# Performance work log

Hardware: AMD Instinct MI355X
Metric: run time of the kernel (lower is better)

## Reference

```python
import jax, jax.numpy as jnp
import numpy as np

B, H, S, D = 4, 16, 2048, 64

def setup_inputs() -> dict:
    key = jax.random.key(0)
    kq, kk, kv = jax.random.split(key, 3)
    q = jax.random.normal(kq, (B, H, S, D), dtype=jnp.float32)
    k = jax.random.normal(kk, (B, H, S, D), dtype=jnp.float32)
    v = jax.random.normal(kv, (B, H, S, D), dtype=jnp.float32)
    return {"q": q, "k": k, "v": v}

def reference(q, k, v):
    # Based linear attention: Taylor-expanded exp kernel, causal, row-sum normalized.
    d = q.shape[-1]
    scale = 1.0 / jnp.sqrt(jnp.asarray(d, dtype=q.dtype))
    s = jnp.einsum('bhqd,bhkd->bhqk', q, k) * scale          # [B,H,S,S]
    p = 1.0 + s + 0.5 * (s * s)                               # Taylor exp approx
    seq = s.shape[-1]
    causal = jnp.tril(jnp.ones((seq, seq), dtype=bool))       # [S,S]
    p = jnp.where(causal, p, 0.0)
    denom = jnp.sum(p, axis=-1, keepdims=True) + 1e-6         # [B,H,S,1]
    out = jnp.einsum('bhqk,bhkd->bhqd', p, v) / denom
    return out
```

## Files before the change

kernel.cpp:

```cpp
#include <hip/hip_runtime.h>
#include <hip/hip_bf16.h>

#define S_LEN 2048
#define DH    64
#define QB    128
#define KB    64
#define BHN   64
#define NQT   16
#define LDS_STRIDE 72

typedef __attribute__((ext_vector_type(8))) short short8;
typedef __attribute__((ext_vector_type(4))) float f32x4;

union Frag {
  short8   s;
  unsigned u[4];
};

__device__ __forceinline__ unsigned pack2(float a, float b) {
  __hip_bfloat162 h2 = __float22bfloat162_rn(make_float2(a, b));
  unsigned u; __builtin_memcpy(&u, &h2, 4);
  return u;
}

__global__ __launch_bounds__(256, 2)
void repack(const float* __restrict__ Kg, const float* __restrict__ Vg,
            short* __restrict__ ws) {
  const int bt = blockIdx.x;
  const int tid = threadIdx.x;
  const size_t tilebase = (size_t)bt * (64 * 64);
  short* kout = ws + (size_t)bt * 4096;
  short* vout = ws + 8388608 + (size_t)bt * 4096;

#pragma unroll
  for (int it = 0; it < 2; ++it) {
    const int c2 = tid + it * 256;
    const int f = c2 >> 6, l = c2 & 63;
    const int kkh = f >> 2, hi = (f >> 1) & 1, cc = f & 1;
    const int row = kkh * 32 + hi * 16 + (l & 15);
    const int col = cc * 32 + (l >> 4) * 8;
    const float* src = Kg + tilebase + row * 64 + col;
    float4 a = *(const float4*)src, b = *(const float4*)(src + 4);
    Frag w;
    w.u[0] = pack2(a.x, a.y); w.u[1] = pack2(a.z, a.w);
    w.u[2] = pack2(b.x, b.y); w.u[3] = pack2(b.z, b.w);
    *(short8*)(kout + f * 512 + l * 8) = w.s;
  }

  __shared__ float vt[64 * 65];
#pragma unroll
  for (int it = 0; it < 4; ++it) {
    const int i = tid + it * 256;
    const int r = i >> 4, c4 = i & 15;
    float4 x = *(const float4*)(Vg + tilebase + r * 64 + c4 * 4);
    vt[r * 65 + c4 * 4 + 0] = x.x; vt[r * 65 + c4 * 4 + 1] = x.y;
    vt[r * 65 + c4 * 4 + 2] = x.z; vt[r * 65 + c4 * 4 + 3] = x.w;
  }
  __syncthreads();
#pragma unroll
  for (int it = 0; it < 2; ++it) {
    const int v2 = tid + it * 256;
    const int v = v2 >> 6, l = v2 & 63;
    const int kkh = v >> 2, n = v & 3;
    const int d = n * 16 + (l & 15);
    const int k0c = kkh * 32 + (l >> 4) * 8;
    Frag w;
#pragma unroll
    for (int jj = 0; jj < 4; ++jj)
      w.u[jj] = pack2(vt[(k0c + 2 * jj) * 65 + d], vt[(k0c + 2 * jj + 1) * 65 + d]);
    *(short8*)(vout + v * 512 + l * 8) = w.s;
  }
}

#define GLOAD(t_, T0, T1, T2, T3)                                              \
  do {                                                                         \
    const short* gsrc_ = ((wv < 2) ? Kf : Vf)                                  \
                         + ((size_t)((bh << 5) + (t_)) << 12)                  \
                         + (size_t)((wv & 1) * 4) * 512 + lane * 8;            \
    T0 = *(const short8*)(gsrc_ + 0 * 512);                                    \
    T1 = *(const short8*)(gsrc_ + 1 * 512);                                    \
    T2 = *(const short8*)(gsrc_ + 2 * 512);                                    \
    T3 = *(const short8*)(gsrc_ + 3 * 512);                                    \
  } while (0)

#define DSWRITE(t_, T0, T1, T2, T3)                                            \
  do {                                                                         \
    short* ld_ = &ring[((t_) & 3) * 8192 + ((wv >= 2) ? 4096 : 0)              \
                       + ((wv & 1) * 4) * 512 + lane * 8];                     \
    *(short8*)(ld_ + 0 * 512) = T0;                                            \
    *(short8*)(ld_ + 1 * 512) = T1;                                            \
    *(short8*)(ld_ + 2 * 512) = T2;                                            \
    *(short8*)(ld_ + 3 * 512) = T3;                                            \
  } while (0)

#define COMPUTE_LDS(t_, MASKED_)                                               \
  do {                                                                         \
    const short* tb_ = &ring[((t_) & 3) * 8192];                               \
    short8 kfr[8], vfr[8];                                                     \
    _Pragma("unroll")                                                          \
    for (int f = 0; f < 8; ++f) kfr[f] = *(const short8*)(tb_ + f * 512 + lane * 8); \
    _Pragma("unroll")                                                          \
    for (int f = 0; f < 8; ++f) vfr[f] = *(const short8*)(tb_ + 4096 + f * 512 + lane * 8); \
    const int k0_ = (t_) * KB;                                                 \
    _Pragma("unroll")                                                          \
    for (int kkh = 0; kkh < 2; ++kkh) {                                        \
      const int kk = kkh * 32;                                                 \
      if (!(MASKED_) || (q0 + wv * 32 + 31 >= k0_ + kk)) {                     \
        f32x4 stL[2], stH[2];                                                  \
        _Pragma("unroll")                                                      \
        for (int hq = 0; hq < 2; ++hq) {                                       \
          stL[hq] = (f32x4){0.f, 0.f, 0.f, 0.f};                               \
          stH[hq] = (f32x4){0.f, 0.f, 0.f, 0.f};                               \
          _Pragma("unroll")                                                    \
          for (int c = 0; c < 2; ++c) {                                        \
            stL[hq] = __builtin_amdgcn_mfma_f32_16x16x32_bf16(kfr[kkh * 4 + c],     qf[hq][c].s, stL[hq], 0, 0, 0); \
            stH[hq] = __builtin_amdgcn_mfma_f32_16x16x32_bf16(kfr[kkh * 4 + 2 + c], qf[hq][c].s, stH[hq], 0, 0, 0); \
          }                                                                    \
        }                                                                      \
        unsigned wrd[2][4];                                                    \
        _Pragma("unroll")                                                      \
        for (int hq = 0; hq < 2; ++hq) {                                       \
          const int qrow = q0 + wv * 32 + hq * 16 + qid;                       \
          float pl[4], ph[4];                                                  \
          _Pragma("unroll")                                                    \
          for (int r = 0; r < 4; ++r) {                                        \
            float sl = stL[hq][r], sh = stH[hq][r];                            \
            pl[r] = fmaf(sl, fmaf(sl, 0.5f, 1.0f), 1.0f);                      \
            ph[r] = fmaf(sh, fmaf(sh, 0.5f, 1.0f), 1.0f);                      \
            if (MASKED_) {                                                     \
              if (k0_ + kk + 4 * g + r > qrow)      pl[r] = 0.f;               \
              if (k0_ + kk + 16 + 4 * g + r > qrow) ph[r] = 0.f;               \
            }                                                                  \
          }                                                                    \
          wrd[hq][0] = pack2(pl[0], pl[1]);                                    \
          wrd[hq][1] = pack2(pl[2], pl[3]);                                    \
          wrd[hq][2] = pack2(ph[0], ph[1]);                                    \
          wrd[hq][3] = pack2(ph[2], ph[3]);                                    \
        }                                                                      \
        Frag pa[2];                                                            \
        _Pragma("unroll")                                                      \
        for (int hq = 0; hq < 2; ++hq) {                                       \
          auto sA32 = __builtin_amdgcn_permlane32_swap(wrd[hq][0], wrd[hq][2], false, false); \
          auto sA16 = __builtin_amdgcn_permlane16_swap(sA32[0], sA32[1], false, false);       \
          auto sB32 = __builtin_amdgcn_permlane32_swap(wrd[hq][1], wrd[hq][3], false, false); \
          auto sB16 = __builtin_amdgcn_permlane16_swap(sB32[0], sB32[1], false, false);       \
          pa[hq].u[0] = (unsigned)sA16[0];                                     \
          pa[hq].u[2] = (unsigned)sA16[1];                                     \
          pa[hq].u[1] = (unsigned)sB16[0];                                     \
          pa[hq].u[3] = (unsigned)sB16[1];                                     \
        }                                                                      \
        _Pragma("unroll")                                                      \
        for (int n = 0; n < 4; ++n) {                                          \
          acc[0][n] = __builtin_amdgcn_mfma_f32_16x16x32_bf16(pa[0].s, vfr[kkh * 4 + n], acc[0][n], 0, 0, 0); \
          acc[1][n] = __builtin_amdgcn_mfma_f32_16x16x32_bf16(pa[1].s, vfr[kkh * 4 + n], acc[1][n], 0, 0, 0); \
        }                                                                      \
        dacc[0] = __builtin_amdgcn_mfma_f32_16x16x32_bf16(pa[0].s, ones.s, dacc[0], 0, 0, 0); \
        dacc[1] = __builtin_amdgcn_mfma_f32_16x16x32_bf16(pa[1].s, ones.s, dacc[1], 0, 0, 0); \
      }                                                                        \
    }                                                                          \
  } while (0)

__global__ __launch_bounds__(256, 2)
void based_lds(const float* __restrict__ Qg, const short* __restrict__ Fr,
               float* __restrict__ Og) {
  const int tid  = threadIdx.x;
  const int lane = tid & 63;
  const int wv   = tid >> 6;
  const int qid  = lane & 15;
  const int g    = lane >> 4;

  const int bh = blockIdx.x;
  const int qy = blockIdx.y;

  __shared__ __align__(16) short ring[4 * 8192];

  const short* Kf = Fr;
  const short* Vf = Fr + 8388608;
  const size_t base = (size_t)bh * S_LEN;

  Frag ones;
  {
    const unsigned ov = (qid == 0) ? 0x3F803F80u : 0u;
    ones.u[0] = ov; ones.u[1] = ov; ones.u[2] = ov; ones.u[3] = ov;
  }

  short8 a0, a1, a2, a3;
  short8 b0, b1, b2, b3;
  short8 c0, c1, c2, c3;

#pragma unroll 1
  for (int half = 0; half < 2; ++half) {
    const int qt = half ? (NQT - 1 - qy) : qy;
    const int q0 = qt * QB;

    Frag qf[2][2];
    {
      const float SC = 0.125f;
#pragma unroll
      for (int hq = 0; hq < 2; ++hq) {
        const int qrow = q0 + wv * 32 + hq * 16 + qid;
        const float* qp = Qg + (base + qrow) * DH + g * 8;
#pragma unroll
        for (int c = 0; c < 2; ++c) {
          float4 f0 = *(const float4*)(qp + c * 32);
          float4 f1 = *(const float4*)(qp + c * 32 + 4);
          qf[hq][c].u[0] = pack2(f0.x * SC, f0.y * SC);
          qf[hq][c].u[1] = pack2(f0.z * SC, f0.w * SC);
          qf[hq][c].u[2] = pack2(f1.x * SC, f1.y * SC);
          qf[hq][c].u[3] = pack2(f1.z * SC, f1.w * SC);
        }
      }
    }

    f32x4 acc[2][4];
    f32x4 dacc[2];
#pragma unroll
    for (int hq = 0; hq < 2; ++hq) {
      dacc[hq] = (f32x4){0.f, 0.f, 0.f, 0.f};
#pragma unroll
      for (int n = 0; n < 4; ++n) acc[hq][n] = (f32x4){0.f, 0.f, 0.f, 0.f};
    }

    const int nfull = 2 * qt;
    const int nt    = nfull + 2;

    __syncthreads();
    GLOAD(0, a0, a1, a2, a3);
    GLOAD(1, b0, b1, b2, b3);
    if (nt > 2) GLOAD(2, c0, c1, c2, c3);
    DSWRITE(0, a0, a1, a2, a3);
    DSWRITE(1, b0, b1, b2, b3);
    if (nt > 2) DSWRITE(2, c0, c1, c2, c3);
    __syncthreads();

    for (int t = 0; t < nfull; ++t) {
      const bool st = (t + 3 < nt);
      if (st) GLOAD(t + 3, a0, a1, a2, a3);
      COMPUTE_LDS(t, 0);
      if (st) DSWRITE(t + 3, a0, a1, a2, a3);
      __syncthreads();
    }

    COMPUTE_LDS(nfull, 1);
    COMPUTE_LDS(nfull + 1, 1);

#pragma unroll
    for (int hq = 0; hq < 2; ++hq) {
#pragma unroll
      for (int r = 0; r < 4; ++r) {
        float dn  = __shfl(dacc[hq][r], 16 * g);
        float inv = 1.0f / (dn + 1e-6f);
        const int row = q0 + wv * 32 + hq * 16 + 4 * g + r;
        float* op = Og + (base + row) * DH + qid;
#pragma unroll
        for (int n = 0; n < 4; ++n) op[n * 16] = acc[hq][n][r] * inv;
      }
    }
  }
}

#define STAGE_LOAD(k0_)                                                        \
  do {                                                                         \
    if (tid < 128) {                                                           \
      const float4* ksrc = (const float4*)(Kg + (base + (size_t)(k0_)) * DH); \
      r0 = ksrc[tid];       r1 = ksrc[tid + 128];                              \
      r2 = ksrc[tid + 256]; r3 = ksrc[tid + 384];                              \
      r4 = ksrc[tid + 512]; r5 = ksrc[tid + 640];                              \
      r6 = ksrc[tid + 768]; r7 = ksrc[tid + 896];                              \
    } else {                                                                   \
      const float4* vsrc = (const float4*)(Vg + (base + (size_t)(k0_)) * DH)  \
                           + ((tid - 128) >> 4) * 128 + ((tid - 128) & 15);    \
      r0 = vsrc[0];  r1 = vsrc[16]; r2 = vsrc[32]; r3 = vsrc[48];              \
      r4 = vsrc[64]; r5 = vsrc[80]; r6 = vsrc[96]; r7 = vsrc[112];             \
    }                                                                          \
  } while (0)

#define STAGE_WRITE(b_)                                                        \
  do {                                                                         \
    if (tid < 128) {                                                           \
      short* Kd = Klds[b_];                                                    \
      const int rb = tid >> 4, c4 = tid & 15;                                  \
      *(uint2*)&Kd[(rb + 0)  * LDS_STRIDE + c4 * 4] = make_uint2(pack2(r0.x, r0.y), pack2(r0.z, r0.w)); \
      *(uint2*)&Kd[(rb + 8)  * LDS_STRIDE + c4 * 4] = make_uint2(pack2(r1.x, r1.y), pack2(r1.z, r1.w)); \
      *(uint2*)&Kd[(rb + 16) * LDS_STRIDE + c4 * 4] = make_uint2(pack2(r2.x, r2.y), pack2(r2.z, r2.w)); \
      *(uint2*)&Kd[(rb + 24) * LDS_STRIDE + c4 * 4] = make_uint2(pack2(r3.x, r3.y), pack2(r3.z, r3.w)); \
      *(uint2*)&Kd[(rb + 32) * LDS_STRIDE + c4 * 4] = make_uint2(pack2(r4.x, r4.y), pack2(r4.z, r4.w)); \
      *(uint2*)&Kd[(rb + 40) * LDS_STRIDE + c4 * 4] = make_uint2(pack2(r5.x, r5.y), pack2(r5.z, r5.w)); \
      *(uint2*)&Kd[(rb + 48) * LDS_STRIDE + c4 * 4] = make_uint2(pack2(r6.x, r6.y), pack2(r6.z, r6.w)); \
      *(uint2*)&Kd[(rb + 56) * LDS_STRIDE + c4 * 4] = make_uint2(pack2(r7.x, r7.y), pack2(r7.z, r7.w)); \
    } else {                                                                   \
      short* Vd = Vlds[b_];                                                    \
      const int l = tid - 128, c4 = l & 15, rp = l >> 4;                       \
      const int slot = (rp + (c4 & 7)) & 7;                                    \
      short* vp = &Vd[(c4 * 4) * LDS_STRIDE + slot * 8];                       \
      Frag w;                                                                  \
      w.u[0] = pack2(r0.x, r1.x); w.u[1] = pack2(r2.x, r3.x);                  \
      w.u[2] = pack2(r4.x, r5.x); w.u[3] = pack2(r6.x, r7.x);                  \
      *(short8*)&vp[0 * LDS_STRIDE] = w.s;                                     \
      w.u[0] = pack2(r0.y, r1.y); w.u[1] = pack2(r2.y, r3.y);                  \
      w.u[2] = pack2(r4.y, r5.y); w.u[3] = pack2(r6.y, r7.y);                  \
      *(short8*)&vp[1 * LDS_STRIDE] = w.s;                                     \
      w.u[0] = pack2(r0.z, r1.z); w.u[1] = pack2(r2.z, r3.z);                  \
      w.u[2] = pack2(r4.z, r5.z); w.u[3] = pack2(r6.z, r7.z);                  \
      *(short8*)&vp[2 * LDS_STRIDE] = w.s;                                     \
      w.u[0] = pack2(r0.w, r1.w); w.u[1] = pack2(r2.w, r3.w);                  \
      w.u[2] = pack2(r4.w, r5.w); w.u[3] = pack2(r6.w, r7.w);                  \
      *(short8*)&vp[3 * LDS_STRIDE] = w.s;                                     \
    }                                                                          \
  } while (0)

#define COMPUTE_TILE(KbP_, VbP_, k0_, MASKED_)                                 \
  do {                                                                         \
    const short* Kb = (KbP_);                                                  \
    const short* Vb = (VbP_);                                                  \
    _Pragma("unroll")                                                          \
    for (int kk = 0; kk < KB; kk += 32) {                                      \
      if (!(MASKED_) || (q0 + wv * 32 + 31 >= (k0_) + kk)) {                   \
        short8 aLo[2], aHi[2];                                                 \
        _Pragma("unroll")                                                      \
        for (int c = 0; c < 2; ++c) {                                          \
          aLo[c] = *(const short8*)&Kb[(kk + qid) * LDS_STRIDE + c * 32 + g * 8];        \
          aHi[c] = *(const short8*)&Kb[(kk + 16 + qid) * LDS_STRIDE + c * 32 + g * 8];   \
        }                                                                      \
        f32x4 stL[2], stH[2];                                                  \
        _Pragma("unroll")                                                      \
        for (int hq = 0; hq < 2; ++hq) {                                       \
          stL[hq] = (f32x4){0.f, 0.f, 0.f, 0.f};                               \
          stH[hq] = (f32x4){0.f, 0.f, 0.f, 0.f};                               \
          _Pragma("unroll")                                                    \
          for (int c = 0; c < 2; ++c) {                                        \
            stL[hq] = __builtin_amdgcn_mfma_f32_16x16x32_bf16(aLo[c], qf[hq][c].s, stL[hq], 0, 0, 0); \
            stH[hq] = __builtin_amdgcn_mfma_f32_16x16x32_bf16(aHi[c], qf[hq][c].s, stH[hq], 0, 0, 0); \
          }                                                                    \
        }                                                                      \
        unsigned wrd[2][4];                                                    \
        _Pragma("unroll")                                                      \
        for (int hq = 0; hq < 2; ++hq) {                                       \
          const int qrow = q0 + wv * 32 + hq * 16 + qid;                       \
          float pl[4], ph[4];                                                  \
          _Pragma("unroll")                                                    \
          for (int r = 0; r < 4; ++r) {                                        \
            float sl = stL[hq][r], sh = stH[hq][r];                            \
            pl[r] = fmaf(sl, fmaf(sl, 0.5f, 1.0f), 1.0f);                      \
            ph[r] = fmaf(sh, fmaf(sh, 0.5f, 1.0f), 1.0f);                      \
            if (MASKED_) {                                                     \
              if ((k0_) + kk + 4 * g + r > qrow)      pl[r] = 0.f;             \
              if ((k0_) + kk + 16 + 4 * g + r > qrow) ph[r] = 0.f;             \
            }                                                                  \
          }                                                                    \
          wrd[hq][0] = pack2(pl[0], pl[1]);                                    \
          wrd[hq][1] = pack2(pl[2], pl[3]);                                    \
          wrd[hq][2] = pack2(ph[0], ph[1]);                                    \
          wrd[hq][3] = pack2(ph[2], ph[3]);                                    \
        }                                                                      \
        Frag pa[2];                                                            \
        _Pragma("unroll")                                                      \
        for (int hq = 0; hq < 2; ++hq) {                                       \
          auto sA32 = __builtin_amdgcn_permlane32_swap(wrd[hq][0], wrd[hq][2], false, false); \
          auto sA16 = __builtin_amdgcn_permlane16_swap(sA32[0], sA32[1], false, false);       \
          auto sB32 = __builtin_amdgcn_permlane32_swap(wrd[hq][1], wrd[hq][3], false, false); \
          auto sB16 = __builtin_amdgcn_permlane16_swap(sB32[0], sB32[1], false, false);       \
          pa[hq].u[0] = (unsigned)sA16[0];                                     \
          pa[hq].u[2] = (unsigned)sA16[1];                                     \
          pa[hq].u[1] = (unsigned)sB16[0];                                     \
          pa[hq].u[3] = (unsigned)sB16[1];                                     \
        }                                                                      \
        _Pragma("unroll")                                                      \
        for (int n = 0; n < 4; ++n) {                                          \
          const int row = n * 16 + qid;                                        \
          const int un  = ((kk >> 3) + g + ((row >> 2) & 7)) & 7;              \
          short8 vb = *(const short8*)&Vb[row * LDS_STRIDE + un * 8];          \
          acc[0][n] = __builtin_amdgcn_mfma_f32_16x16x32_bf16(pa[0].s, vb, acc[0][n], 0, 0, 0); \
          acc[1][n] = __builtin_amdgcn_mfma_f32_16x16x32_bf16(pa[1].s, vb, acc[1][n], 0, 0, 0); \
        }                                                                      \
        dacc[0] = __builtin_amdgcn_mfma_f32_16x16x32_bf16(pa[0].s, ones.s, dacc[0], 0, 0, 0);   \
        dacc[1] = __builtin_amdgcn_mfma_f32_16x16x32_bf16(pa[1].s, ones.s, dacc[1], 0, 0, 0);   \
      }                                                                        \
    }                                                                          \
  } while (0)

__global__ __launch_bounds__(256, 2)
void based_attn(const float* __restrict__ Qg,
                const float* __restrict__ Kg,
                const float* __restrict__ Vg,
                float* __restrict__ Og) {
  const int tid  = threadIdx.x;
  const int lane = tid & 63;
  const int wv   = tid >> 6;
  const int qid  = lane & 15;
  const int g    = lane >> 4;

  const int bh = blockIdx.x;
  const int qy = blockIdx.y;

  __shared__ short Klds[2][KB * LDS_STRIDE];
  __shared__ short Vlds[2][DH * LDS_STRIDE];

  const size_t base = (size_t)bh * S_LEN;

  Frag ones;
  {
    const unsigned ov = (qid == 0) ? 0x3F803F80u : 0u;
    ones.u[0] = ov; ones.u[1] = ov; ones.u[2] = ov; ones.u[3] = ov;
  }

  float4 r0, r1, r2, r3, r4, r5, r6, r7;

#pragma unroll 1
  for (int half = 0; half < 2; ++half) {
    const int qt = half ? (NQT - 1 - qy) : qy;
    const int q0 = qt * QB;

    Frag qf[2][2];
    {
      const float SC = 0.125f;
#pragma unroll
      for (int hq = 0; hq < 2; ++hq) {
        const int qrow = q0 + wv * 32 + hq * 16 + qid;
        const float* qp = Qg + (base + qrow) * DH + g * 8;
#pragma unroll
        for (int c = 0; c < 2; ++c) {
          float4 f0 = *(const float4*)(qp + c * 32);
          float4 f1 = *(const float4*)(qp + c * 32 + 4);
          qf[hq][c].u[0] = pack2(f0.x * SC, f0.y * SC);
          qf[hq][c].u[1] = pack2(f0.z * SC, f0.w * SC);
          qf[hq][c].u[2] = pack2(f1.x * SC, f1.y * SC);
          qf[hq][c].u[3] = pack2(f1.z * SC, f1.w * SC);
        }
      }
    }

    f32x4 acc[2][4];
    f32x4 dacc[2];
#pragma unroll
    for (int hq = 0; hq < 2; ++hq) {
      dacc[hq] = (f32x4){0.f, 0.f, 0.f, 0.f};
#pragma unroll
      for (int n = 0; n < 4; ++n) acc[hq][n] = (f32x4){0.f, 0.f, 0.f, 0.f};
    }

    STAGE_LOAD(0);
    STAGE_WRITE(0);
    __syncthreads();

    const int nfull = 2 * qt;
    for (int t = 0; t < nfull; ++t) {
      STAGE_LOAD((t + 1) * KB);
      COMPUTE_TILE(Klds[t & 1], Vlds[t & 1], t * KB, 0);
      STAGE_WRITE((t + 1) & 1);
      __syncthreads();
    }
    {
      int t = nfull;
      STAGE_LOAD((t + 1) * KB);
      COMPUTE_TILE(Klds[t & 1], Vlds[t & 1], t * KB, 1);
      STAGE_WRITE((t + 1) & 1);
      __syncthreads();
      t = nfull + 1;
      COMPUTE_TILE(Klds[t & 1], Vlds[t & 1], t * KB, 1);
    }

#pragma unroll
    for (int hq = 0; hq < 2; ++hq) {
#pragma unroll
      for (int r = 0; r < 4; ++r) {
        float dn  = __shfl(dacc[hq][r], 16 * g);
        float inv = 1.0f / (dn + 1e-6f);
        const int row = q0 + wv * 32 + hq * 16 + 4 * g + r;
        float* op = Og + (base + row) * DH + qid;
#pragma unroll
        for (int n = 0; n < 4; ++n) op[n * 16] = acc[hq][n][r] * inv;
      }
    }
  }
}

extern "C" void kernel_launch(void* const* d_in, const int* in_sizes, int n_in,
                              void* d_out, int out_size, void* d_ws, size_t ws_size,
                              hipStream_t stream) {
  (void)in_sizes; (void)n_in; (void)out_size;
  const float* Q = (const float*)d_in[0];
  const float* K = (const float*)d_in[1];
  const float* V = (const float*)d_in[2];
  float* O = (float*)d_out;

  if (ws_size >= (size_t)33554432) {
    short* ws = (short*)d_ws;
    repack<<<dim3(2048), 256, 0, stream>>>(K, V, ws);
    based_lds<<<dim3(64, 8), 256, 0, stream>>>(Q, ws, O);
  } else {
    dim3 grid(BHN, NQT / 2);
    based_attn<<<grid, 256, 0, stream>>>(Q, K, V, O);
  }
}
```

Measured before the change: 69.53 us.

## Process paired low and high query tiles in one shared K/V sweep

Each block used to handle its two query tiles (qy and NQT-1-qy) one after the other, streaming the K/V prefix twice. Now both tiles' Q fragments and accumulators stay live together, so the K/V tiles for the low tile's range are loaded once and used by both tiles. This cuts repeated global and LDS traffic and pipeline refills. In exchange it roughly doubles accumulator and Q-fragment registers per wave, which may cause spills or lower occupancy under launch_bounds(256,2).

```diff
diff --git a/kernel.cpp b/kernel.cpp
--- a/kernel.cpp
+++ b/kernel.cpp
@@ -93,76 +93,97 @@
     *(short8*)(ld_ + 3 * 512) = T3;                                            \
   } while (0)
 
-#define COMPUTE_LDS(t_, MASKED_)                                               \
+#define QBODY(QF, ACC, DACC, Q0_, MASKED_)                                     \
+  if (!(MASKED_) || (Q0_ + wv * 32 + 31 >= k0_ + kk)) {                        \
+    f32x4 stL[2], stH[2];                                                      \
+    _Pragma("unroll")                                                          \
+    for (int hq = 0; hq < 2; ++hq) {                                           \
+      stL[hq] = (f32x4){0.f, 0.f, 0.f, 0.f};                                   \
+      stH[hq] = (f32x4){0.f, 0.f, 0.f, 0.f};                                   \
+      _Pragma("unroll")                                                        \
+      for (int c = 0; c < 2; ++c) {                                            \
+        stL[hq] = __builtin_amdgcn_mfma_f32_16x16x32_bf16(kf[c],     QF[hq][c].s, stL[hq], 0, 0, 0); \
+        stH[hq] = __builtin_amdgcn_mfma_f32_16x16x32_bf16(kf[2 + c], QF[hq][c].s, stH[hq], 0, 0, 0); \
+      }                                                                        \
+    }                                                                          \
+    unsigned wrd[2][4];                                                        \
+    _Pragma("unroll")                                                          \
+    for (int hq = 0; hq < 2; ++hq) {                                           \
+      const int qrow = Q0_ + wv * 32 + hq * 16 + qid;                          \
+      float pl[4], ph[4];                                                      \
+      _Pragma("unroll")                                                        \
+      for (int r = 0; r < 4; ++r) {                                            \
+        float sl = stL[hq][r], sh = stH[hq][r];                                \
+        pl[r] = fmaf(sl, fmaf(sl, 0.5f, 1.0f), 1.0f);                          \
+        ph[r] = fmaf(sh, fmaf(sh, 0.5f, 1.0f), 1.0f);                          \
+        if (MASKED_) {                                                         \
+          if (k0_ + kk + 4 * g + r > qrow)      pl[r] = 0.f;                   \
+          if (k0_ + kk + 16 + 4 * g + r > qrow) ph[r] = 0.f;                   \
+        }                                                                      \
+      }                                                                        \
+      wrd[hq][0] = pack2(pl[0], pl[1]);                                        \
+      wrd[hq][1] = pack2(pl[2], pl[3]);                                        \
+      wrd[hq][2] = pack2(ph[0], ph[1]);                                        \
+      wrd[hq][3] = pack2(ph[2], ph[3]);                                        \
+    }                                                                          \
+    Frag pa[2];                                                                \
+    _Pragma("unroll")                                                          \
+    for (int hq = 0; hq < 2; ++hq) {                                           \
+      auto sA32 = __builtin_amdgcn_permlane32_swap(wrd[hq][0], wrd[hq][2], false, false); \
+      auto sA16 = __builtin_amdgcn_permlane16_swap(sA32[0], sA32[1], false, false);       \
+      auto sB32 = __builtin_amdgcn_permlane32_swap(wrd[hq][1], wrd[hq][3], false, false); \
+      auto sB16 = __builtin_amdgcn_permlane16_swap(sB32[0], sB32[1], false, false);       \
+      pa[hq].u[0] = (unsigned)sA16[0];                                         \
+      pa[hq].u[2] = (unsigned)sA16[1];                                         \
+      pa[hq].u[1] = (unsigned)sB16[0];                                         \
+      pa[hq].u[3] = (unsigned)sB16[1];                                         \
+    }                                                                          \
+    _Pragma("unroll")                                                          \
+    for (int n = 0; n < 4; ++n) {                                              \
+      ACC[0][n] = __builtin_amdgcn_mfma_f32_16x16x32_bf16(pa[0].s, vf[n], ACC[0][n], 0, 0, 0); \
+      ACC[1][n] = __builtin_amdgcn_mfma_f32_16x16x32_bf16(pa[1].s, vf[n], ACC[1][n], 0, 0, 0); \
+    }                                                                          \
+    DACC[0] = __builtin_amdgcn_mfma_f32_16x16x32_bf16(pa[0].s, ones.s, DACC[0], 0, 0, 0); \
+    DACC[1] = __builtin_amdgcn_mfma_f32_16x16x32_bf16(pa[1].s, ones.s, DACC[1], 0, 0, 0); \
+  }
+
+#define PHASE(t_, DOLO, MLO, MHI)                                              \
   do {                                                                         \
     const short* tb_ = &ring[((t_) & 3) * 8192];                               \
-    short8 kfr[8], vfr[8];                                                     \
-    _Pragma("unroll")                                                          \
-    for (int f = 0; f < 8; ++f) kfr[f] = *(const short8*)(tb_ + f * 512 + lane * 8); \
-    _Pragma("unroll")                                                          \
-    for (int f = 0; f < 8; ++f) vfr[f] = *(const short8*)(tb_ + 4096 + f * 512 + lane * 8); \
     const int k0_ = (t_) * KB;                                                 \
     _Pragma("unroll")                                                          \
     for (int kkh = 0; kkh < 2; ++kkh) {                                        \
       const int kk = kkh * 32;                                                 \
-      if (!(MASKED_) || (q0 + wv * 32 + 31 >= k0_ + kk)) {                     \
-        f32x4 stL[2], stH[2];                                                  \
+      short8 kf[4], vf[4];                                                     \
+      _Pragma("unroll")                                                        \
+      for (int j = 0; j < 4; ++j) {                                            \
+        kf[j] = *(const short8*)(tb_ + (kkh * 4 + j) * 512 + lane * 8);        \
+        vf[j] = *(const short8*)(tb_ + 4096 + (kkh * 4 + j) * 512 + lane * 8); \
+      }                                                                        \
+      if (DOLO) { QBODY(qfL, accL, daccL, q0L, MLO) }                          \
+      QBODY(qfR, accR, daccR, q0R, MHI)                                        \
+    }                                                                          \
+  } while (0)
+
+#define EPI(ACC, DACC, Q0_)                                                    \
+  do {                                                                         \
+    _Pragma("unroll")                                                          \
+    for (int hq = 0; hq < 2; ++hq) {                                           \
+      _Pragma("unroll")                                                        \
+      for (int r = 0; r < 4; ++r) {                                            \
+        float dn  = __shfl(DACC[hq][r], 16 * g);                               \
+        float inv = 1.0f / (dn + 1e-6f);                                       \
+        const int row = Q0_ + wv * 32 + hq * 16 + 4 * g + r;                   \
+        float* op = Og + (base + row) * DH + qid;                              \
         _Pragma("unroll")                                                      \
-        for (int hq = 0; hq < 2; ++hq) {                                       \
-          stL[hq] = (f32x4){0.f, 0.f, 0.f, 0.f};                               \
-          stH[hq] = (f32x4){0.f, 0.f, 0.f, 0.f};                               \
-          _Pragma("unroll")                                                    \
-          for (int c = 0; c < 2; ++c) {                                        \
-            stL[hq] = __builtin_amdgcn_mfma_f32_16x16x32_bf16(kfr[kkh * 4 + c],     qf[hq][c].s, stL[hq], 0, 0, 0); \
-            stH[hq] = __builtin_amdgcn_mfma_f32_16x16x32_bf16(kfr[kkh * 4 + 2 + c], qf[hq][c].s, stH[hq], 0, 0, 0); \
-          }                                                                    \
-        }                                                                      \
-        unsigned wrd[2][4];                                                    \
-        _Pragma("unroll")                                                      \
-        for (int hq = 0; hq < 2; ++hq) {                                       \
-          const int qrow = q0 + wv * 32 + hq * 16 + qid;                       \
-          float pl[4], ph[4];                                                  \
-          _Pragma("unroll")                                                    \
-          for (int r = 0; r < 4; ++r) {                                        \
-            float sl = stL[hq][r], sh = stH[hq][r];                            \
-            pl[r] = fmaf(sl, fmaf(sl, 0.5f, 1.0f), 1.0f);                      \
-            ph[r] = fmaf(sh, fmaf(sh, 0.5f, 1.0f), 1.0f);                      \
-            if (MASKED_) {                                                     \
-              if (k0_ + kk + 4 * g + r > qrow)      pl[r] = 0.f;               \
-              if (k0_ + kk + 16 + 4 * g + r > qrow) ph[r] = 0.f;               \
-            }                                                                  \
-          }                                                                    \
-          wrd[hq][0] = pack2(pl[0], pl[1]);                                    \
-          wrd[hq][1] = pack2(pl[2], pl[3]);                                    \
-          wrd[hq][2] = pack2(ph[0], ph[1]);                                    \
-          wrd[hq][3] = pack2(ph[2], ph[3]);                                    \
-        }                                                                      \
-        Frag pa[2];                                                            \
-        _Pragma("unroll")                                                      \
-        for (int hq = 0; hq < 2; ++hq) {                                       \
-          auto sA32 = __builtin_amdgcn_permlane32_swap(wrd[hq][0], wrd[hq][2], false, false); \
-          auto sA16 = __builtin_amdgcn_permlane16_swap(sA32[0], sA32[1], false, false);       \
-          auto sB32 = __builtin_amdgcn_permlane32_swap(wrd[hq][1], wrd[hq][3], false, false); \
-          auto sB16 = __builtin_amdgcn_permlane16_swap(sB32[0], sB32[1], false, false);       \
-          pa[hq].u[0] = (unsigned)sA16[0];                                     \
-          pa[hq].u[2] = (unsigned)sA16[1];                                     \
-          pa[hq].u[1] = (unsigned)sB16[0];                                     \
-          pa[hq].u[3] = (unsigned)sB16[1];                                     \
-        }                                                                      \
-        _Pragma("unroll")                                                      \
-        for (int n = 0; n < 4; ++n) {                                          \
-          acc[0][n] = __builtin_amdgcn_mfma_f32_16x16x32_bf16(pa[0].s, vfr[kkh * 4 + n], acc[0][n], 0, 0, 0); \
-          acc[1][n] = __builtin_amdgcn_mfma_f32_16x16x32_bf16(pa[1].s, vfr[kkh * 4 + n], acc[1][n], 0, 0, 0); \
-        }                                                                      \
-        dacc[0] = __builtin_amdgcn_mfma_f32_16x16x32_bf16(pa[0].s, ones.s, dacc[0], 0, 0, 0); \
-        dacc[1] = __builtin_amdgcn_mfma_f32_16x16x32_bf16(pa[1].s, ones.s, dacc[1], 0, 0, 0); \
+        for (int n = 0; n < 4; ++n) op[n * 16] = ACC[hq][n][r] * inv;          \
       }                                                                        \
     }                                                                          \
   } while (0)
 
 __global__ __launch_bounds__(256, 2)
-void based_lds(const float* __restrict__ Qg, const short* __restrict__ Fr,
-               float* __restrict__ Og) {
+void based_dual(const float* __restrict__ Qg, const short* __restrict__ Fr,
+                float* __restrict__ Og) {
   const int tid  = threadIdx.x;
   const int lane = tid & 63;
   const int wv   = tid >> 6;
@@ -171,6 +192,8 @@
 
   const int bh = blockIdx.x;
   const int qy = blockIdx.y;
+  const int qlo = qy, qhi = NQT - 1 - qy;
+  const int q0L = qlo * QB, q0R = qhi * QB;
 
   __shared__ __align__(16) short ring[4 * 8192];
 
@@ -184,79 +207,83 @@
     ones.u[0] = ov; ones.u[1] = ov; ones.u[2] = ov; ones.u[3] = ov;
   }
 
-  short8 a0, a1, a2, a3;
-  short8 b0, b1, b2, b3;
-  short8 c0, c1, c2, c3;
-
-#pragma unroll 1
-  for (int half = 0; half < 2; ++half) {
-    const int qt = half ? (NQT - 1 - qy) : qy;
-    const int q0 = qt * QB;
-
-    Frag qf[2][2];
-    {
-      const float SC = 0.125f;
-#pragma unroll
-      for (int hq = 0; hq < 2; ++hq) {
-        const int qrow = q0 + wv * 32 + hq * 16 + qid;
+  Frag qfL[2][2], qfR[2][2];
+  {
+    const float SC = 0.125f;
+#pragma unroll
+    for (int hq = 0; hq < 2; ++hq) {
+#pragma unroll
+      for (int side = 0; side < 2; ++side) {
+        const int qrow = (side ? q0R : q0L) + wv * 32 + hq * 16 + qid;
         const float* qp = Qg + (base + qrow) * DH + g * 8;
 #pragma unroll
         for (int c = 0; c < 2; ++c) {
           float4 f0 = *(const float4*)(qp + c * 32);
           float4 f1 = *(const float4*)(qp + c * 32 + 4);
-          qf[hq][c].u[0] = pack2(f0.x * SC, f0.y * SC);
-          qf[hq][c].u[1] = pack2(f0.z * SC, f0.w * SC);
-          qf[hq][c].u[2] = pack2(f1.x * SC, f1.y * SC);
-          qf[hq][c].u[3] = pack2(f1.z * SC, f1.w * SC);
+          Frag w;
+          w.u[0] = pack2(f0.x * SC, f0.y * SC);
+          w.u[1] = pack2(f0.z * SC, f0.w * SC);
+          w.u[2] = pack2(f1.x * SC, f1.y * SC);
+          w.u[3] = pack2(f1.z * SC, f1.w * SC);
+          if (side) qfR[hq][c] = w; else qfL[hq][c] = w;
         }
       }
     }
-
-    f32x4 acc[2][4];
-    f32x4 dacc[2];
-#pragma unroll
-    for (int hq = 0; hq < 2; ++hq) {
-      dacc[hq] = (f32x4){0.f, 0.f, 0.f, 0.f};
-#pragma unroll
-      for (int n = 0; n < 4; ++n) acc[hq][n] = (f32x4){0.f, 0.f, 0.f, 0.f};
-    }
-
-    const int nfull = 2 * qt;
-    const int nt    = nfull + 2;
-
+  }
+
+  f32x4 accL[2][4], accR[2][4];
+  f32x4 daccL[2], daccR[2];
+#pragma unroll
+  for (int hq = 0; hq < 2; ++hq) {
+    daccL[hq] = (f32x4){0.f, 0.f, 0.f, 0.f};
+    daccR[hq] = (f32x4){0.f, 0.f, 0.f, 0.f};
+#pragma unroll
+    for (int n = 0; n < 4; ++n) {
+      accL[hq][n] = (f32x4){0.f, 0.f, 0.f, 0.f};
+      accR[hq][n] = (f32x4){0.f, 0.f, 0.f, 0.f};
+    }
+  }
+
+  const int nt = 2 * qhi + 2;
+  const int e1 = 2 * qlo, e2 = 2 * qlo + 2, e3 = 2 * qhi;
+
+  short8 a0, a1, a2, a3, b0, b1, b2, b3, c0, c1, c2, c3;
+
+  GLOAD(0, a0, a1, a2, a3);
+  GLOAD(1, b0, b1, b2, b3);
+  GLOAD(2, c0, c1, c2, c3);
+  DSWRITE(0, a0, a1, a2, a3);
+  DSWRITE(1, b0, b1, b2, b3);
+  DSWRITE(2, c0, c1, c2, c3);
+  __syncthreads();
+
+  int t = 0;
+  for (; t < e1; ++t) {
+    const bool st = (t + 3 < nt);
+    if (st) GLOAD(t + 3, a0, a1, a2, a3);
+    PHASE(t, 1, 0, 0);
+    if (st) DSWRITE(t + 3, a0, a1, a2, a3);
     __syncthreads();
-    GLOAD(0, a0, a1, a2, a3);
-    GLOAD(1, b0, b1, b2, b3);
-    if (nt > 2) GLOAD(2, c0, c1, c2, c3);
-    DSWRITE(0, a0, a1, a2, a3);
-    DSWRITE(1, b0, b1, b2, b3);
-    if (nt > 2) DSWRITE(2, c0, c1, c2, c3);
+  }
+  for (; t < e2; ++t) {
+    const bool st = (t + 3 < nt);
+    if (st) GLOAD(t + 3, a0, a1, a2, a3);
+    PHASE(t, 1, 1, 0);
+    if (st) DSWRITE(t + 3, a0, a1, a2, a3);
     __syncthreads();
-
-    for (int t = 0; t < nfull; ++t) {
-      const bool st = (t + 3 < nt);
-      if (st) GLOAD(t + 3, a0, a1, a2, a3);
-      COMPUTE_LDS(t, 0);
-      if (st) DSWRITE(t + 3, a0, a1, a2, a3);
-      __syncthreads();
-    }
-
-    COMPUTE_LDS(nfull, 1);
-    COMPUTE_LDS(nfull + 1, 1);
-
-#pragma unroll
-    for (int hq = 0; hq < 2; ++hq) {
-#pragma unroll
-      for (int r = 0; r < 4; ++r) {
-        float dn  = __shfl(dacc[hq][r], 16 * g);
-        float inv = 1.0f / (dn + 1e-6f);
-        const int row = q0 + wv * 32 + hq * 16 + 4 * g + r;
-        float* op = Og + (base + row) * DH + qid;
-#pragma unroll
-        for (int n = 0; n < 4; ++n) op[n * 16] = acc[hq][n][r] * inv;
-      }
-    }
-  }
+  }
+  EPI(accL, daccL, q0L);
+  for (; t < e3; ++t) {
+    const bool st = (t + 3 < nt);
+    if (st) GLOAD(t + 3, a0, a1, a2, a3);
+    PHASE(t, 0, 0, 0);
+    if (st) DSWRITE(t + 3, a0, a1, a2, a3);
+    __syncthreads();
+  }
+  for (; t < nt; ++t) {
+    PHASE(t, 0, 0, 1);
+  }
+  EPI(accR, daccR, q0R);
 }
 
 #define STAGE_LOAD(k0_)                                                        \
@@ -487,7 +514,7 @@
   if (ws_size >= (size_t)33554432) {
     short* ws = (short*)d_ws;
     repack<<<dim3(2048), 256, 0, stream>>>(K, V, ws);
-    based_lds<<<dim3(64, 8), 256, 0, stream>>>(Q, ws, O);
+    based_dual<<<dim3(64, 8), 256, 0, stream>>>(Q, ws, O);
   } else {
     dim3 grid(BHN, NQT / 2);
     based_attn<<<grid, 256, 0, stream>>>(Q, K, V, O);
```

After: 68.77 us. No clear change (-1.1%).

## Split attention into one query tile per block with double-buffered LDS ring

Applied to the files above, without the earlier changes.

Each block now handles a single causal query tile instead of a paired light and heavy tile. The grid doubles to 64x16, heaviest tiles are scheduled first, and launch bounds rise to 4 blocks per CU. The LDS ring shrinks from four tile slots to two, prefetch depth drops to one tile, and K/V fragments are loaded per 32-key half to lower register pressure. The Taylor polynomial is rewritten as 1+(1+s)^2 by seeding the score accumulator with ones, which doubles p; doubling the epsilon keeps the normalized output equivalent. The shallower prefetch may expose more global-load latency, which the higher occupancy is meant to hide.

```diff
diff --git a/kernel.cpp b/kernel.cpp
--- a/kernel.cpp
+++ b/kernel.cpp
@@ -85,7 +85,7 @@
 
 #define DSWRITE(t_, T0, T1, T2, T3)                                            \
   do {                                                                         \
-    short* ld_ = &ring[((t_) & 3) * 8192 + ((wv >= 2) ? 4096 : 0)              \
+    short* ld_ = &ring[((t_) & 1) * 8192 + ((wv >= 2) ? 4096 : 0)              \
                        + ((wv & 1) * 4) * 512 + lane * 8];                     \
     *(short8*)(ld_ + 0 * 512) = T0;                                            \
     *(short8*)(ld_ + 1 * 512) = T1;                                            \
@@ -93,28 +93,29 @@
     *(short8*)(ld_ + 3 * 512) = T3;                                            \
   } while (0)
 
-#define COMPUTE_LDS(t_, MASKED_)                                               \
-  do {                                                                         \
-    const short* tb_ = &ring[((t_) & 3) * 8192];                               \
-    short8 kfr[8], vfr[8];                                                     \
-    _Pragma("unroll")                                                          \
-    for (int f = 0; f < 8; ++f) kfr[f] = *(const short8*)(tb_ + f * 512 + lane * 8); \
-    _Pragma("unroll")                                                          \
-    for (int f = 0; f < 8; ++f) vfr[f] = *(const short8*)(tb_ + 4096 + f * 512 + lane * 8); \
+#define PHASE(t_, MASKED_)                                                     \
+  do {                                                                         \
+    const short* tb_ = &ring[((t_) & 1) * 8192];                               \
     const int k0_ = (t_) * KB;                                                 \
     _Pragma("unroll")                                                          \
     for (int kkh = 0; kkh < 2; ++kkh) {                                        \
       const int kk = kkh * 32;                                                 \
       if (!(MASKED_) || (q0 + wv * 32 + 31 >= k0_ + kk)) {                     \
+        short8 kf[4], vf[4];                                                   \
+        _Pragma("unroll")                                                      \
+        for (int j = 0; j < 4; ++j) {                                          \
+          kf[j] = *(const short8*)(tb_ + (kkh * 4 + j) * 512 + lane * 8);      \
+          vf[j] = *(const short8*)(tb_ + 4096 + (kkh * 4 + j) * 512 + lane * 8); \
+        }                                                                      \
         f32x4 stL[2], stH[2];                                                  \
         _Pragma("unroll")                                                      \
         for (int hq = 0; hq < 2; ++hq) {                                       \
-          stL[hq] = (f32x4){0.f, 0.f, 0.f, 0.f};                               \
-          stH[hq] = (f32x4){0.f, 0.f, 0.f, 0.f};                               \
+          stL[hq] = onesf;                                                     \
+          stH[hq] = onesf;                                                     \
           _Pragma("unroll")                                                    \
           for (int c = 0; c < 2; ++c) {                                        \
-            stL[hq] = __builtin_amdgcn_mfma_f32_16x16x32_bf16(kfr[kkh * 4 + c],     qf[hq][c].s, stL[hq], 0, 0, 0); \
-            stH[hq] = __builtin_amdgcn_mfma_f32_16x16x32_bf16(kfr[kkh * 4 + 2 + c], qf[hq][c].s, stH[hq], 0, 0, 0); \
+            stL[hq] = __builtin_amdgcn_mfma_f32_16x16x32_bf16(kf[c],     qf[hq][c].s, stL[hq], 0, 0, 0); \
+            stH[hq] = __builtin_amdgcn_mfma_f32_16x16x32_bf16(kf[2 + c], qf[hq][c].s, stH[hq], 0, 0, 0); \
           }                                                                    \
         }                                                                      \
         unsigned wrd[2][4];                                                    \
@@ -124,9 +125,9 @@
           float pl[4], ph[4];                                                  \
           _Pragma("unroll")                                                    \
           for (int r = 0; r < 4; ++r) {                                        \
-            float sl = stL[hq][r], sh = stH[hq][r];                            \
-            pl[r] = fmaf(sl, fmaf(sl, 0.5f, 1.0f), 1.0f);                      \
-            ph[r] = fmaf(sh, fmaf(sh, 0.5f, 1.0f), 1.0f);                      \
+            float tl = stL[hq][r], th = stH[hq][r];                            \
+            pl[r] = fmaf(tl, tl, 1.0f);             \
+            ph[r] = fmaf(th, th, 1.0f);                                        \
             if (MASKED_) {                                                     \
               if (k0_ + kk + 4 * g + r > qrow)      pl[r] = 0.f;               \
               if (k0_ + kk + 16 + 4 * g + r > qrow) ph[r] = 0.f;               \
@@ -151,8 +152,8 @@
         }                                                                      \
         _Pragma("unroll")                                                      \
         for (int n = 0; n < 4; ++n) {                                          \
-          acc[0][n] = __builtin_amdgcn_mfma_f32_16x16x32_bf16(pa[0].s, vfr[kkh * 4 + n], acc[0][n], 0, 0, 0); \
-          acc[1][n] = __builtin_amdgcn_mfma_f32_16x16x32_bf16(pa[1].s, vfr[kkh * 4 + n], acc[1][n], 0, 0, 0); \
+          acc[0][n] = __builtin_amdgcn_mfma_f32_16x16x32_bf16(pa[0].s, vf[n], acc[0][n], 0, 0, 0); \
+          acc[1][n] = __builtin_amdgcn_mfma_f32_16x16x32_bf16(pa[1].s, vf[n], acc[1][n], 0, 0, 0); \
         }                                                                      \
         dacc[0] = __builtin_amdgcn_mfma_f32_16x16x32_bf16(pa[0].s, ones.s, dacc[0], 0, 0, 0); \
         dacc[1] = __builtin_amdgcn_mfma_f32_16x16x32_bf16(pa[1].s, ones.s, dacc[1], 0, 0, 0); \
@@ -160,8 +161,8 @@
     }                                                                          \
   } while (0)
 
-__global__ __launch_bounds__(256, 2)
-void based_lds(const float* __restrict__ Qg, const short* __restrict__ Fr,
+__global__ __launch_bounds__(256, 4)
+void based_one(const float* __restrict__ Qg, const short* __restrict__ Fr,
                float* __restrict__ Og) {
   const int tid  = threadIdx.x;
   const int lane = tid & 63;
@@ -170,9 +171,10 @@
   const int g    = lane >> 4;
 
   const int bh = blockIdx.x;
-  const int qy = blockIdx.y;
-
-  __shared__ __align__(16) short ring[4 * 8192];
+  const int qt = NQT - 1 - (int)blockIdx.y;
+  const int q0 = qt * QB;
+
+  __shared__ __align__(16) short ring[2 * 8192];
 
   const short* Kf = Fr;
   const short* Vf = Fr + 8388608;
@@ -183,78 +185,66 @@
     const unsigned ov = (qid == 0) ? 0x3F803F80u : 0u;
     ones.u[0] = ov; ones.u[1] = ov; ones.u[2] = ov; ones.u[3] = ov;
   }
+  const f32x4 onesf = (f32x4){1.f, 1.f, 1.f, 1.f};
+
+  Frag qf[2][2];
+  {
+    const float SC = 0.125f;
+#pragma unroll
+    for (int hq = 0; hq < 2; ++hq) {
+      const int qrow = q0 + wv * 32 + hq * 16 + qid;
+      const float* qp = Qg + (base + qrow) * DH + g * 8;
+#pragma unroll
+      for (int c = 0; c < 2; ++c) {
+        float4 f0 = *(const float4*)(qp + c * 32);
+        float4 f1 = *(const float4*)(qp + c * 32 + 4);
+        qf[hq][c].u[0] = pack2(f0.x * SC, f0.y * SC);
+        qf[hq][c].u[1] = pack2(f0.z * SC, f0.w * SC);
+        qf[hq][c].u[2] = pack2(f1.x * SC, f1.y * SC);
+        qf[hq][c].u[3] = pack2(f1.z * SC, f1.w * SC);
+      }
+    }
+  }
+
+  f32x4 acc[2][4];
+  f32x4 dacc[2];
+#pragma unroll
+  for (int hq = 0; hq < 2; ++hq) {
+    dacc[hq] = (f32x4){0.f, 0.f, 0.f, 0.f};
+#pragma unroll
+    for (int n = 0; n < 4; ++n) acc[hq][n] = (f32x4){0.f, 0.f, 0.f, 0.f};
+  }
+
+  const int nfull = 2 * qt;
 
   short8 a0, a1, a2, a3;
-  short8 b0, b1, b2, b3;
-  short8 c0, c1, c2, c3;
-
-#pragma unroll 1
-  for (int half = 0; half < 2; ++half) {
-    const int qt = half ? (NQT - 1 - qy) : qy;
-    const int q0 = qt * QB;
-
-    Frag qf[2][2];
-    {
-      const float SC = 0.125f;
-#pragma unroll
-      for (int hq = 0; hq < 2; ++hq) {
-        const int qrow = q0 + wv * 32 + hq * 16 + qid;
-        const float* qp = Qg + (base + qrow) * DH + g * 8;
-#pragma unroll
-        for (int c = 0; c < 2; ++c) {
-          float4 f0 = *(const float4*)(qp + c * 32);
-          float4 f1 = *(const float4*)(qp + c * 32 + 4);
-          qf[hq][c].u[0] = pack2(f0.x * SC, f0.y * SC);
-          qf[hq][c].u[1] = pack2(f0.z * SC, f0.w * SC);
-          qf[hq][c].u[2] = pack2(f1.x * SC, f1.y * SC);
-          qf[hq][c].u[3] = pack2(f1.z * SC, f1.w * SC);
-        }
-      }
-    }
-
-    f32x4 acc[2][4];
-    f32x4 dacc[2];
-#pragma unroll
-    for (int hq = 0; hq < 2; ++hq) {
-      dacc[hq] = (f32x4){0.f, 0.f, 0.f, 0.f};
-#pragma unroll
-      for (int n = 0; n < 4; ++n) acc[hq][n] = (f32x4){0.f, 0.f, 0.f, 0.f};
-    }
-
-    const int nfull = 2 * qt;
-    const int nt    = nfull + 2;
-
+
+  GLOAD(0, a0, a1, a2, a3);
+  DSWRITE(0, a0, a1, a2, a3);
+  __syncthreads();
+
+  for (int t = 0; t < nfull; ++t) {
+    GLOAD(t + 1, a0, a1, a2, a3);
+    PHASE(t, 0);
+    DSWRITE(t + 1, a0, a1, a2, a3);
     __syncthreads();
-    GLOAD(0, a0, a1, a2, a3);
-    GLOAD(1, b0, b1, b2, b3);
-    if (nt > 2) GLOAD(2, c0, c1, c2, c3);
-    DSWRITE(0, a0, a1, a2, a3);
-    DSWRITE(1, b0, b1, b2, b3);
-    if (nt > 2) DSWRITE(2, c0, c1, c2, c3);
-    __syncthreads();
-
-    for (int t = 0; t < nfull; ++t) {
-      const bool st = (t + 3 < nt);
-      if (st) GLOAD(t + 3, a0, a1, a2, a3);
-      COMPUTE_LDS(t, 0);
-      if (st) DSWRITE(t + 3, a0, a1, a2, a3);
-      __syncthreads();
-    }
-
-    COMPUTE_LDS(nfull, 1);
-    COMPUTE_LDS(nfull + 1, 1);
-
-#pragma unroll
-    for (int hq = 0; hq < 2; ++hq) {
-#pragma unroll
-      for (int r = 0; r < 4; ++r) {
-        float dn  = __shfl(dacc[hq][r], 16 * g);
-        float inv = 1.0f / (dn + 1e-6f);
-        const int row = q0 + wv * 32 + hq * 16 + 4 * g + r;
-        float* op = Og + (base + row) * DH + qid;
-#pragma unroll
-        for (int n = 0; n < 4; ++n) op[n * 16] = acc[hq][n][r] * inv;
-      }
+  }
+  GLOAD(nfull + 1, a0, a1, a2, a3);
+  PHASE(nfull, 1);
+  DSWRITE(nfull + 1, a0, a1, a2, a3);
+  __syncthreads();
+  PHASE(nfull + 1, 1);
+
+#pragma unroll
+  for (int hq = 0; hq < 2; ++hq) {
+#pragma unroll
+    for (int r = 0; r < 4; ++r) {
+      float dn  = __shfl(dacc[hq][r], 16 * g);
+      float inv = 1.0f / (dn + 2e-6f);
+      const int row = q0 + wv * 32 + hq * 16 + 4 * g + r;
+      float* op = Og + (base + row) * DH + qid;
+#pragma unroll
+      for (int n = 0; n < 4; ++n) op[n * 16] = acc[hq][n][r] * inv;
     }
   }
 }
@@ -487,7 +477,7 @@
   if (ws_size >= (size_t)33554432) {
     short* ws = (short*)d_ws;
     repack<<<dim3(2048), 256, 0, stream>>>(K, V, ws);
-    based_lds<<<dim3(64, 8), 256, 0, stream>>>(Q, ws, O);
+    based_one<<<dim3(64, 16), 256, 0, stream>>>(Q, ws, O);
   } else {
     dim3 grid(BHN, NQT / 2);
     based_attn<<<grid, 256, 0, stream>>>(Q, K, V, O);
```

Result: faster. 64.72 us (-6.9%).
